# Kernel optimization log

Measured on AMD Instinct MI355X. Metric: run time of the kernel, lower is better.

## Reference

```python
import jax, jax.numpy as jnp
import numpy as np

B, D, C, F = 1024, 8192, 345, 512
PROTO_W = 0.99  # args.proto_m


def setup_inputs() -> dict:
    key = jax.random.key(0)
    k = jax.random.split(key, 6)
    img_q = jax.random.normal(k[0], (B, D), jnp.float32)
    img_q1 = jax.random.normal(k[1], (B, D), jnp.float32)
    # partial label mask: random candidate set, guarantee >=1 candidate per row
    partial_Y = (jax.random.uniform(k[2], (B, C)) < 0.3).astype(jnp.float32)
    partial_Y = partial_Y.at[jnp.arange(B), jnp.arange(B) % C].set(1.0)
    W_enc = jax.random.normal(k[3], (D, F), jnp.float32) / np.sqrt(D).astype(np.float32)
    W_fc = jax.random.normal(k[4], (F, C), jnp.float32) / np.sqrt(F).astype(np.float32)
    b_fc = jnp.zeros((C,), jnp.float32)
    proto = jax.random.normal(k[5], (C, F), jnp.float32)
    proto = proto / jnp.linalg.norm(proto, axis=1, keepdims=True)
    return {"img_q": img_q, "img_q1": img_q1, "partial_Y": partial_Y,
            "W_enc": W_enc, "W_fc": W_fc, "b_fc": b_fc, "proto": proto}


def reference(img_q, img_q1, partial_Y, W_enc, W_fc, b_fc, proto):
    # encoder: feats [B,F], logits [B,C] (abstracted backbone + shared fc)
    feats_q = img_q @ W_enc
    logits_q = feats_q @ W_fc + b_fc
    feats_q1 = img_q1 @ W_enc
    logits_q1 = feats_q1 @ W_fc + b_fc

    # partial-label restricted pseudo labels
    scores = jax.nn.softmax(logits_q, axis=1) * partial_Y
    scores = scores / scores.sum(axis=1, keepdims=True)
    labels = jnp.argmax(scores, axis=1)  # [B] int

    # Sequential per-sample EMA p[l] = w*p[l] + (1-w)*f, vectorized in closed form.
    # For a sample with c_after same-label samples occurring later, its final
    # contribution is (1-w)*w^c_after * f; the old prototype is scaled by w^count.
    onehot = jax.nn.one_hot(labels, C, dtype=feats_q.dtype)   # [B,C]
    cum = jnp.cumsum(onehot, axis=0)                          # inclusive counts
    occ = cum[jnp.arange(B), labels] - 1.0                    # occurrences before i
    total = cum[-1]                                           # [C] per-class counts
    c_after = total[labels] - occ - 1.0                       # [B]
    coef = (1.0 - PROTO_W) * PROTO_W ** c_after               # [B]
    contrib = jax.ops.segment_sum(coef[:, None] * feats_q, labels, num_segments=C)
    new_proto = (PROTO_W ** total)[:, None] * proto + contrib
    new_proto = new_proto / jnp.linalg.norm(new_proto, axis=1, keepdims=True)

    prot_scores = new_proto @ W_fc + b_fc
    return logits_q, logits_q1, new_proto, prot_scores, labels, feats_q, feats_q1
```

## Files before the change

kernel.cpp:

```cpp
#include <hip/hip_runtime.h>
#include <float.h>
#include <math.h>

#define B_SZ 1024
#define D_SZ 8192
#define C_SZ 345
#define F_SZ 512
#define PROTO_W 0.99f


#define WS_XH 0
#define WS_XL 33554432u
#define WS_WH 67108864u
#define WS_WL 75497472u
#define WS_P  83886080u
#define WS2_WFH 100663296u
#define WS2_WFL 101056512u
#define WS2_LAB 101449728u
#define WS2_NEED 101457920u

#define WS_NEED 92274688u
#define WS_FH  0u
#define WS_FL  2097152u
#define WS_WFH 4194304u
#define WS_WFL 4587520u
#define WS_NPH 4980736u
#define WS_NPL 5373952u

typedef short bf16x8 __attribute__((ext_vector_type(8)));
typedef short short4v __attribute__((ext_vector_type(4)));
typedef short short8v __attribute__((ext_vector_type(8)));
typedef float f32x4  __attribute__((ext_vector_type(4)));

__device__ __forceinline__ void split_bf16(float x, short& hi, short& lo) {
    unsigned u = __float_as_uint(x);
    unsigned r = (u + 0x7FFFu + ((u >> 16) & 1u)) >> 16;
    hi = (short)r;
    float hf = __uint_as_float(r << 16);
    lo = (short)(__float_as_uint(x - hf) >> 16);
}
__device__ __forceinline__ float bf16_f32(short h) {
    return __uint_as_float(((unsigned)(unsigned short)h) << 16);
}

__device__ __forceinline__ void gl_lds16(const short* g, short* l) {
    __builtin_amdgcn_global_load_lds(
        (const __attribute__((address_space(1))) void*)g,
        (__attribute__((address_space(3))) void*)l, 16, 0, 0);
}

__device__ __forceinline__ unsigned f2key(float v) {
    unsigned u = __float_as_uint(v);
    return (u & 0x80000000u) ? ~u : (u | 0x80000000u);
}

__device__ __forceinline__ void fence_barrier() {
    asm volatile("" ::: "memory");
    __builtin_amdgcn_s_barrier();
    asm volatile("" ::: "memory");
}

#define MFMA_BF16 __builtin_amdgcn_mfma_f32_16x16x32_bf16

#define MFMA_BLOCK(IA0, IA1, IB0, IB1)                                   \
    do {                                                                 \
        bf16x8 a0h = *(const bf16x8*)&sAh[IA0];                          \
        bf16x8 a1h = *(const bf16x8*)&sAh[IA1];                          \
        bf16x8 b0h = *(const bf16x8*)&sBh[IB0];                          \
        bf16x8 b1h = *(const bf16x8*)&sBh[IB1];                          \
        bf16x8 a0l = *(const bf16x8*)&sAl[IA0];                          \
        bf16x8 a1l = *(const bf16x8*)&sAl[IA1];                          \
        bf16x8 b0l = *(const bf16x8*)&sBl[IB0];                          \
        bf16x8 b1l = *(const bf16x8*)&sBl[IB1];                          \
        acc[0][0] = MFMA_BF16(a0h, b0h, acc[0][0], 0, 0, 0);             \
        acc[0][1] = MFMA_BF16(a0h, b1h, acc[0][1], 0, 0, 0);             \
        acc[1][0] = MFMA_BF16(a1h, b0h, acc[1][0], 0, 0, 0);             \
        acc[1][1] = MFMA_BF16(a1h, b1h, acc[1][1], 0, 0, 0);             \
        acc[0][0] = MFMA_BF16(a0h, b0l, acc[0][0], 0, 0, 0);             \
        acc[0][1] = MFMA_BF16(a0h, b1l, acc[0][1], 0, 0, 0);             \
        acc[1][0] = MFMA_BF16(a1h, b0l, acc[1][0], 0, 0, 0);             \
        acc[1][1] = MFMA_BF16(a1h, b1l, acc[1][1], 0, 0, 0);             \
        acc[0][0] = MFMA_BF16(a0l, b0h, acc[0][0], 0, 0, 0);             \
        acc[0][1] = MFMA_BF16(a0l, b1h, acc[0][1], 0, 0, 0);             \
        acc[1][0] = MFMA_BF16(a1l, b0h, acc[1][0], 0, 0, 0);             \
        acc[1][1] = MFMA_BF16(a1l, b1h, acc[1][1], 0, 0, 0);             \
    } while (0)


__global__ __launch_bounds__(256) void convert_pack2(
    const float* __restrict__ img_q, const float* __restrict__ img_q1,
    const float* __restrict__ W_enc, const float* __restrict__ W_fc,
    short* __restrict__ Ahp, short* __restrict__ Alp,
    short* __restrict__ Bhp, short* __restrict__ Blp,
    short* __restrict__ Wth, short* __restrict__ Wtl,
    unsigned long long* __restrict__ labPack)
{
    __shared__ float tile[64][65];
    const int bid = blockIdx.x;
    const int t = threadIdx.x;

    if (bid < 4)
        labPack[bid * 256 + t] = 0ull;

    if (bid < 1024) {
        const int total = 2048 * 1024;
        for (int i = bid * 256 + t; i < total; i += 1024 * 256) {
            const int row = i >> 10;
            const int cc = i & 1023;
            const float* src = (row < B_SZ)
                ? &img_q[(size_t)row * D_SZ + cc * 8]
                : &img_q1[(size_t)(row - B_SZ) * D_SZ + cc * 8];
            float4 a = ((const float4*)src)[0];
            float4 b = ((const float4*)src)[1];
            float f[8] = {a.x, a.y, a.z, a.w, b.x, b.y, b.z, b.w};
            short8v h, l;
#pragma unroll
            for (int e = 0; e < 8; ++e) {
                short hh, ll;
                split_bf16(f[e], hh, ll);
                h[e] = hh; l[e] = ll;
            }
            const int mt = row >> 7;
            const int pr = row & 127;
            const int kstep = cc >> 2;
            const int c = cc & 3;
            const int hf = pr >> 6;
            const int r = pr & 63;
            const int rp = r >> 1;
            const int slot = (((r & 1) << 2) | c) ^ (rp & 7);
            const size_t dst = (size_t)(mt * 256 + kstep) * 4096
                             + hf * 2048 + rp * 64 + slot * 8;
            *(short8v*)&Ahp[dst] = h;
            *(short8v*)&Alp[dst] = l;
        }
    } else if (bid < 2048) {
        const int id = bid - 1024;
        const int kstep64 = id >> 3;
        const int k0 = kstep64 * 64;
        const int n0 = (id & 7) * 64;
        {
            const int kr = t >> 2;
            const int cb = (t & 3) * 16;
#pragma unroll
            for (int j = 0; j < 4; ++j) {
                float4 v = *(const float4*)&W_enc[(size_t)(k0 + kr) * F_SZ + n0 + cb + j * 4];
                tile[kr][cb + j * 4 + 0] = v.x;
                tile[kr][cb + j * 4 + 1] = v.y;
                tile[kr][cb + j * 4 + 2] = v.z;
                tile[kr][cb + j * 4 + 3] = v.w;
            }
        }
        __syncthreads();
        const int n = t >> 2;
#pragma unroll
        for (int cc2 = 0; cc2 < 2; ++cc2) {
            const int ch = (t & 3) * 2 + cc2;
            short8v h, l;
#pragma unroll
            for (int e = 0; e < 8; ++e) {
                short hh, ll;
                split_bf16(tile[ch * 8 + e][n], hh, ll);
                h[e] = hh; l[e] = ll;
            }
            const int nrow = n0 + n;
            const int k32 = kstep64 * 2 + (ch >> 2);
            const int c = ch & 3;
            const int nt_ = nrow >> 7;
            const int pr = nrow & 127;
            const int hf = pr >> 6;
            const int r = pr & 63;
            const int rp = r >> 1;
            const int slot = (((r & 1) << 2) | c) ^ (rp & 7);
            const size_t dst = (size_t)(nt_ * 256 + k32) * 4096
                             + hf * 2048 + rp * 64 + slot * 8;
            *(short8v*)&Bhp[dst] = h;
            *(short8v*)&Blp[dst] = l;
        }
    } else {
        const int id = bid - 2048;
        const int k0 = (id & 7) * 64;
        const int c0 = (id >> 3) * 64;
        for (int idx = t; idx < 64 * 64; idx += 256) {
            const int kr = idx >> 6;
            const int cc = idx & 63;
            tile[kr][cc] = (c0 + cc < C_SZ) ? W_fc[(size_t)(k0 + kr) * C_SZ + c0 + cc] : 0.0f;
        }
        __syncthreads();
        const int crow = t >> 2;
#pragma unroll
        for (int cc2 = 0; cc2 < 2; ++cc2) {
            const int ch = (t & 3) * 2 + cc2;
            short8v h, l;
#pragma unroll
            for (int e = 0; e < 8; ++e) {
                short hh, ll;
                split_bf16(tile[ch * 8 + e][crow], hh, ll);
                h[e] = hh; l[e] = ll;
            }
            size_t off = (size_t)(c0 + crow) * F_SZ + k0 + ch * 8;
            *(short8v*)&Wth[off] = h;
            *(short8v*)&Wtl[off] = l;
        }
    }
}

#define V5_MFMA(PAH, PAL, PBH, PBL)                                          \
    do {                                                                     \
        bf16x8 ah[4], al[4], bh_[2], bl_[2];                                 \
        _Pragma("unroll")                                                    \
        for (int f = 0; f < 4; ++f) {                                        \
            ah[f] = *(const bf16x8*)&(PAH)[aoff[f]];                         \
            al[f] = *(const bf16x8*)&(PAL)[aoff[f]];                         \
        }                                                                    \
        _Pragma("unroll")                                                    \
        for (int g = 0; g < 2; ++g) {                                        \
            bh_[g] = *(const bf16x8*)&(PBH)[boff[g]];                        \
            bl_[g] = *(const bf16x8*)&(PBL)[boff[g]];                        \
        }                                                                    \
        __builtin_amdgcn_s_setprio(1);                                       \
        _Pragma("unroll")                                                    \
        for (int f = 0; f < 4; ++f)                                          \
            _Pragma("unroll")                                                \
            for (int g = 0; g < 2; ++g)                                      \
                acc[f][g] = MFMA_BF16(ah[f], bh_[g], acc[f][g], 0, 0, 0);    \
        _Pragma("unroll")                                                    \
        for (int f = 0; f < 4; ++f)                                          \
            _Pragma("unroll")                                                \
            for (int g = 0; g < 2; ++g)                                      \
                acc[f][g] = MFMA_BF16(ah[f], bl_[g], acc[f][g], 0, 0, 0);    \
        _Pragma("unroll")                                                    \
        for (int f = 0; f < 4; ++f)                                          \
            _Pragma("unroll")                                                \
            for (int g = 0; g < 2; ++g)                                      \
                acc[f][g] = MFMA_BF16(al[f], bh_[g], acc[f][g], 0, 0, 0);    \
        __builtin_amdgcn_s_setprio(0);                                       \
    } while (0)

#define V5_STEP(BI, SD, SW, VMLIT)                                           \
    do {                                                                     \
        asm volatile("s_waitcnt vmcnt(" VMLIT ")" ::: "memory");             \
        fence_barrier();                                                     \
        {                                                                    \
            const short* gg = gsrc0 + (size_t)(SW) * 4096;                   \
            gl_lds16(gg, SD);                                                \
            gl_lds16(gg + 512, (SD) + 512);                                  \
            gl_lds16(gg + 1024, (SD) + 1024);                                \
            gl_lds16(gg + 1536, (SD) + 1536);                                \
        }                                                                    \
        V5_MFMA(SAh[BI], SAl[BI], SBh[BI], SBl[BI]);                         \
    } while (0)

#define V5_STEPN(BI, VMLIT)                                                  \
    do {                                                                     \
        asm volatile("s_waitcnt vmcnt(" VMLIT ")" ::: "memory");             \
        fence_barrier();                                                     \
        V5_MFMA(SAh[BI], SAl[BI], SBh[BI], SBl[BI]);                         \
    } while (0)

__global__ __launch_bounds__(512, 1) void gemm_ws128_v5(
    const short* __restrict__ Ahp, const short* __restrict__ Alp,
    const short* __restrict__ Bhp, const short* __restrict__ Blp,
    float* __restrict__ P)
{
    __shared__ __align__(16) short SAh[4][4096];
    __shared__ __align__(16) short SAl[4][4096];
    __shared__ __align__(16) short SBh[4][4096];
    __shared__ __align__(16) short SBl[4][4096];

    const int t = threadIdx.x;
    const int lane = t & 63;
    const int wave = t >> 6;

    const int flat = blockIdx.x + 4 * blockIdx.y + 64 * blockIdx.z;
    const int logical = (flat & 7) * 32 + (flat >> 3);
    const int nt = logical & 3;
    const int mt = (logical >> 2) & 15;
    const int ks = logical >> 6;

    const int m0 = mt * 128;
    const int n0 = nt * 128;

    const int arr = wave >> 1;
    const int half = wave & 1;
    const short* gtile =
        (arr == 0) ? Ahp + (size_t)(mt * 256) * 4096 :
        (arr == 1) ? Alp + (size_t)(mt * 256) * 4096 :
        (arr == 2) ? Bhp + (size_t)(nt * 256) * 4096 :
                     Blp + (size_t)(nt * 256) * 4096;
    const short* gsrc0 = gtile + (size_t)(ks * 64) * 4096 + half * 2048 + lane * 8;

    short* abase =
        (arr == 0) ? &SAh[0][0] : (arr == 1) ? &SAl[0][0] :
        (arr == 2) ? &SBh[0][0] : &SBl[0][0];
    short* sd0 = abase + 0 * 4096 + half * 2048;
    short* sd1 = abase + 1 * 4096 + half * 2048;
    short* sd2 = abase + 2 * 4096 + half * 2048;
    short* sd3 = abase + 3 * 4096 + half * 2048;

    const int wr = wave >> 2;
    const int wc = wave & 3;
    const int mo = wr * 64;
    const int no = wc * 32;
    const int lr = lane & 15;
    const int lkg = lane >> 4;
    int aoff[4], boff[2];
#pragma unroll
    for (int f = 0; f < 4; ++f) {
        const int R = mo + 16 * f + lr;
        const int r = R & 63;
        const int rp = r >> 1;
        aoff[f] = (R >> 6) * 2048 + rp * 64
                + (((((r & 1) << 2) | lkg)) ^ (rp & 7)) * 8;
    }
#pragma unroll
    for (int g = 0; g < 2; ++g) {
        const int R = no + 16 * g + lr;
        const int r = R & 63;
        const int rp = r >> 1;
        boff[g] = (R >> 6) * 2048 + rp * 64
                + (((((r & 1) << 2) | lkg)) ^ (rp & 7)) * 8;
    }

    f32x4 acc[4][2] = {};

    {
        gl_lds16(gsrc0,        sd0);
        gl_lds16(gsrc0 + 512,  sd0 + 512);
        gl_lds16(gsrc0 + 1024, sd0 + 1024);
        gl_lds16(gsrc0 + 1536, sd0 + 1536);
        const short* g1 = gsrc0 + 4096;
        gl_lds16(g1,        sd1);
        gl_lds16(g1 + 512,  sd1 + 512);
        gl_lds16(g1 + 1024, sd1 + 1024);
        gl_lds16(g1 + 1536, sd1 + 1536);
        const short* g2 = gsrc0 + 8192;
        gl_lds16(g2,        sd2);
        gl_lds16(g2 + 512,  sd2 + 512);
        gl_lds16(g2 + 1024, sd2 + 1024);
        gl_lds16(g2 + 1536, sd2 + 1536);
    }

    for (int s4 = 0; s4 < 15; ++s4) {
        const int sb = s4 * 4;
        V5_STEP(0, sd3, sb + 3, "8");
        V5_STEP(1, sd0, sb + 4, "8");
        V5_STEP(2, sd1, sb + 5, "8");
        V5_STEP(3, sd2, sb + 6, "8");
    }
    V5_STEP (0, sd3, 63, "8");
    V5_STEPN(1, "8");
    V5_STEPN(2, "4");
    V5_STEPN(3, "0");

    float* Pout = P + (size_t)ks * (2048u * 512u);
#pragma unroll
    for (int f = 0; f < 4; ++f)
#pragma unroll
        for (int g = 0; g < 2; ++g) {
            const int col  = n0 + no + 16 * g + (lane & 15);
            const int row0 = m0 + mo + 16 * f + (lane >> 4) * 4;
#pragma unroll
            for (int r = 0; r < 4; ++r)
                Pout[(size_t)(row0 + r) * F_SZ + col] = acc[f][g][r];
        }
}

__global__ __launch_bounds__(256) void reduce_feats4(
    const float* __restrict__ P, float* __restrict__ feats,
    short* __restrict__ Fh, short* __restrict__ Fl)
{
    const int i4 = blockIdx.x * 256 + threadIdx.x;
    float4 a = ((const float4*)P)[i4];
#pragma unroll
    for (int sl = 1; sl < 4; ++sl) {
        float4 b = ((const float4*)(P + (size_t)sl * (2048u * 512u)))[i4];
        a.x += b.x; a.y += b.y; a.z += b.z; a.w += b.w;
    }
    ((float4*)feats)[i4] = a;
    float v[4] = {a.x, a.y, a.z, a.w};
    short4v h, l;
    short hh, ll;
#pragma unroll
    for (int e = 0; e < 4; ++e) {
        split_bf16(v[e], hh, ll); h[e] = hh; l[e] = ll;
    }
    ((short4v*)Fh)[i4] = h;
    ((short4v*)Fl)[i4] = l;
}

__global__ __launch_bounds__(256, 2) void fc_logits3(
    const short* __restrict__ Ah, const short* __restrict__ Al,
    const short* __restrict__ Bh_g, const short* __restrict__ Bl_g,
    const float* __restrict__ bias, const float* __restrict__ partial_Y,
    float* __restrict__ logits, unsigned long long* __restrict__ labPack)
{
    __shared__ __align__(16) short dAh[2][4096];
    __shared__ __align__(16) short dAl[2][4096];
    __shared__ __align__(16) short dBh[2][4096];
    __shared__ __align__(16) short dBl[2][4096];

    const int t = threadIdx.x;
    const int lane = t & 63;
    const int wave = t >> 6;
    const int n0 = blockIdx.x * 64;
    const int m0 = blockIdx.y * 64;

    const int lrow8 = lane >> 3;
    const int colOff = ((lane & 7) ^ lrow8) * 8;

    const short* gsrc = (wave == 0) ? Ah : (wave == 1) ? Al
                      : (wave == 2) ? Bh_g : Bl_g;
    const int rbase = (wave < 2) ? m0 : n0;
    short* lb[2];
    lb[0] = (wave == 0) ? dAh[0] : (wave == 1) ? dAl[0] : (wave == 2) ? dBh[0] : dBl[0];
    lb[1] = (wave == 0) ? dAh[1] : (wave == 1) ? dAl[1] : (wave == 2) ? dBh[1] : dBl[1];
    const short* gbase = gsrc + (size_t)(rbase + lrow8) * F_SZ + colOff;

    const int mo = (wave >> 1) * 32;
    const int no = (wave & 1) * 32;
    const int lr = lane & 15;
    const int lkg = lane >> 4;
    const int x7 = lr & 7;
    const int sl0 = (0 + lkg) ^ x7;
    const int sl1 = (4 + lkg) ^ x7;
    const int ra0 = (mo + lr) * 64,      ra1 = (mo + 16 + lr) * 64;
    const int rb0 = (no + lr) * 64,      rb1 = (no + 16 + lr) * 64;
    const int a00 = ra0 + sl0 * 8, a01 = ra0 + sl1 * 8;
    const int a10 = ra1 + sl0 * 8, a11 = ra1 + sl1 * 8;
    const int b00 = rb0 + sl0 * 8, b01 = rb0 + sl1 * 8;
    const int b10 = rb1 + sl0 * 8, b11 = rb1 + sl1 * 8;

    f32x4 acc[2][2] = {};

#pragma unroll
    for (int j = 0; j < 8; ++j)
        gl_lds16(gbase + (size_t)(8 * j) * F_SZ, lb[0] + j * 512);

    int buf = 0;
    for (int s = 0; s < 8; ++s) {
        if (s + 1 < 8) {
            short* dst = lb[buf ^ 1];
            const short* g = gbase + (s + 1) * 64;
#pragma unroll
            for (int j = 0; j < 8; ++j)
                gl_lds16(g + (size_t)(8 * j) * F_SZ, dst + j * 512);
            asm volatile("s_waitcnt vmcnt(8)" ::: "memory");
        } else {
            asm volatile("s_waitcnt vmcnt(0)" ::: "memory");
        }
        fence_barrier();
        __builtin_amdgcn_s_setprio(1);
        {
            const short* sAh = dAh[buf];
            const short* sAl = dAl[buf];
            const short* sBh = dBh[buf];
            const short* sBl = dBl[buf];
            MFMA_BLOCK(a00, a10, b00, b10);
            MFMA_BLOCK(a01, a11, b01, b11);
        }
        __builtin_amdgcn_s_setprio(0);
        fence_barrier();
        buf ^= 1;
    }

    const bool doArg = (m0 < B_SZ);
#pragma unroll
    for (int f = 0; f < 2; ++f) {
#pragma unroll
        for (int r = 0; r < 4; ++r) {
            const int row = m0 + mo + f * 16 + (lane >> 4) * 4 + r;
            unsigned long long best = 0;
#pragma unroll
            for (int g = 0; g < 2; ++g) {
                const int col = n0 + no + g * 16 + (lane & 15);
                if (col < C_SZ) {
                    const float v = acc[f][g][r] + bias[col];
                    logits[(size_t)row * C_SZ + col] = v;
                    if (doArg && partial_Y[(size_t)row * C_SZ + col] != 0.0f) {
                        unsigned long long p = ((unsigned long long)f2key(v) << 32)
                                             | (unsigned long long)(0xFFFFFFFFu - (unsigned)col);
                        if (p > best) best = p;
                    }
                }
            }
            if (doArg) {
#pragma unroll
                for (int m = 1; m < 16; m <<= 1) {
                    unsigned long long o = __shfl_xor(best, m);
                    if (o > best) best = o;
                }
                if ((lane & 15) == 0 && best != 0)
                    atomicMax(&labPack[row], best);
            }
        }
    }
}

__global__ __launch_bounds__(512) void proto_scores_fused(
    const unsigned long long* __restrict__ labPack,
    const float* __restrict__ feats_q,
    const float* __restrict__ proto,
    const short* __restrict__ Wth, const short* __restrict__ Wtl,
    const float* __restrict__ b_fc,
    float* __restrict__ new_proto, float* __restrict__ scores,
    float* __restrict__ labels_f)
{
    __shared__ int rowlist[B_SZ];
    __shared__ int mcount_s;
    __shared__ float nprow[F_SZ];
    __shared__ float red[8];
    __shared__ float rinv_s;
    const int c = blockIdx.x;
    const int t = threadIdx.x;
    const int lane = t & 63;
    const int w = t >> 6;

    if (c == 0) {
#pragma unroll
        for (int j = 0; j < 2; ++j) {
            const int i = t + j * 512;
            int li = (int)(0xFFFFFFFFu - (unsigned)(labPack[i] & 0xFFFFFFFFull));
            labels_f[i] = (float)li;
        }
    }

    if (w == 0) {
        int k = 0;
#pragma unroll
        for (int ch = 0; ch < 16; ++ch) {
            unsigned long long pk = labPack[ch * 64 + lane];
            int li = (int)(0xFFFFFFFFu - (unsigned)(pk & 0xFFFFFFFFull));
            unsigned long long mask = __ballot(li == c);
            if (lane == 0) {
                while (mask) {
                    int p = __builtin_ctzll(mask);
                    mask &= mask - 1;
                    rowlist[k++] = ch * 64 + p;
                }
            }
            k = __shfl(k, 0);
        }
        if (lane == 0) mcount_s = k;
    }
    __syncthreads();
    const int m = mcount_s;

    float val = proto[(size_t)c * F_SZ + t];
    for (int k = 0; k < m; ++k)
        val = PROTO_W * val + (1.0f - PROTO_W) * feats_q[(size_t)rowlist[k] * F_SZ + t];

    float sq = val * val;
#pragma unroll
    for (int off = 32; off; off >>= 1) sq += __shfl_down(sq, off);
    if ((t & 63) == 0) red[t >> 6] = sq;
    __syncthreads();
    if (t == 0) {
        float s = 0.0f;
#pragma unroll
        for (int ww = 0; ww < 8; ++ww) s += red[ww];
        rinv_s = 1.0f / sqrtf(s);
    }
    __syncthreads();
    const float v = val * rinv_s;
    new_proto[(size_t)c * F_SZ + t] = v;
    nprow[t] = v;
    __syncthreads();

    float np8[8];
#pragma unroll
    for (int j = 0; j < 8; ++j) np8[j] = nprow[lane * 8 + j];
    for (int col = w; col < C_SZ; col += 8) {
        const short8v h = *(const short8v*)&Wth[(size_t)col * F_SZ + lane * 8];
        const short8v l = *(const short8v*)&Wtl[(size_t)col * F_SZ + lane * 8];
        float p = 0.0f;
#pragma unroll
        for (int j = 0; j < 8; ++j)
            p += np8[j] * (bf16_f32(h[j]) + bf16_f32(l[j]));
#pragma unroll
        for (int off = 32; off; off >>= 1) p += __shfl_down(p, off);
        if (lane == 0) scores[(size_t)c * C_SZ + col] = p + b_fc[col];
    }
}

__global__ __launch_bounds__(256) void convert_all(
    const float* __restrict__ img_q, const float* __restrict__ img_q1,
    const float* __restrict__ W_enc, const float* __restrict__ W_fc,
    short* __restrict__ Xh, short* __restrict__ Xl,
    short* __restrict__ Wh, short* __restrict__ Wl,
    short* __restrict__ Wth, short* __restrict__ Wtl,
    unsigned long long* __restrict__ labPack)
{
    __shared__ float tile[64][65];
    const int bid = blockIdx.x;
    const int t = threadIdx.x;

    if (labPack && bid < 4)
        labPack[bid * 256 + t] = 0ull;

    if (bid < 1024) {
        const int HALF = (B_SZ * D_SZ) / 4;
        const int total = 2 * HALF;
        for (int i4 = bid * 256 + t; i4 < total; i4 += 1024 * 256) {
            float4 v = (i4 < HALF) ? ((const float4*)img_q)[i4]
                                   : ((const float4*)img_q1)[i4 - HALF];
            short4v h, l;
            short hh, ll;
            split_bf16(v.x, hh, ll); h.x = hh; l.x = ll;
            split_bf16(v.y, hh, ll); h.y = hh; l.y = ll;
            split_bf16(v.z, hh, ll); h.z = hh; l.z = ll;
            split_bf16(v.w, hh, ll); h.w = hh; l.w = ll;
            ((short4v*)Xh)[i4] = h;
            ((short4v*)Xl)[i4] = l;
        }
    } else if (bid < 2048) {
        const int id = bid - 1024;
        const int k0 = (id >> 3) * 64;
        const int n0 = (id & 7) * 64;
        {
            const int kr = t >> 2;
            const int cb = (t & 3) * 16;
#pragma unroll
            for (int j = 0; j < 4; ++j) {
                float4 v = *(const float4*)&W_enc[(size_t)(k0 + kr) * F_SZ + n0 + cb + j * 4];
                tile[kr][cb + j * 4 + 0] = v.x;
                tile[kr][cb + j * 4 + 1] = v.y;
                tile[kr][cb + j * 4 + 2] = v.z;
                tile[kr][cb + j * 4 + 3] = v.w;
            }
        }
        __syncthreads();
        const int n = t >> 2;
#pragma unroll
        for (int cc = 0; cc < 2; ++cc) {
            const int ch = (t & 3) * 2 + cc;
            short8v h, l;
#pragma unroll
            for (int e = 0; e < 8; ++e) {
                short hh, ll;
                split_bf16(tile[ch * 8 + e][n], hh, ll);
                h[e] = hh; l[e] = ll;
            }
            size_t off = (size_t)(n0 + n) * D_SZ + k0 + ch * 8;
            *(short8v*)&Wh[off] = h;
            *(short8v*)&Wl[off] = l;
        }
    } else {
        const int id = bid - 2048;
        const int k0 = (id & 7) * 64;
        const int c0 = (id >> 3) * 64;
        for (int idx = t; idx < 64 * 64; idx += 256) {
            const int kr = idx >> 6;
            const int cc = idx & 63;
            tile[kr][cc] = (c0 + cc < C_SZ) ? W_fc[(size_t)(k0 + kr) * C_SZ + c0 + cc] : 0.0f;
        }
        __syncthreads();
        const int crow = t >> 2;
#pragma unroll
        for (int cc2 = 0; cc2 < 2; ++cc2) {
            const int ch = (t & 3) * 2 + cc2;
            short8v h, l;
#pragma unroll
            for (int e = 0; e < 8; ++e) {
                short hh, ll;
                split_bf16(tile[ch * 8 + e][crow], hh, ll);
                h[e] = hh; l[e] = ll;
            }
            size_t off = (size_t)(c0 + crow) * F_SZ + k0 + ch * 8;
            *(short8v*)&Wth[off] = h;
            *(short8v*)&Wtl[off] = l;
        }
    }
}

__global__ __launch_bounds__(256, 1) void gemm_ws128(
    const short* __restrict__ Xh, const short* __restrict__ Xl,
    const short* __restrict__ Wh, const short* __restrict__ Wl,
    float* __restrict__ P, int ksteps)
{
    __shared__ __align__(16) short sAh[2][8192];
    __shared__ __align__(16) short sAl[2][8192];
    __shared__ __align__(16) short sBh[2][8192];
    __shared__ __align__(16) short sBl[2][8192];

    const int t = threadIdx.x;
    const int lane = t & 63;
    const int wave = t >> 6;
    const int nt = blockIdx.x;
    const int mt = blockIdx.y;
    const int ks = blockIdx.z;
    const int m0 = mt * 128;
    const int n0 = nt * 128;
    const int kbase = ks * ksteps * 64;

    const short* gbase =
        (wave == 0) ? Xh + (size_t)m0 * D_SZ :
        (wave == 1) ? Xl + (size_t)m0 * D_SZ :
        (wave == 2) ? Wh + (size_t)n0 * D_SZ :
                      Wl + (size_t)n0 * D_SZ;
    short* lb[2];
    lb[0] = (wave == 0) ? sAh[0] : (wave == 1) ? sAl[0] : (wave == 2) ? sBh[0] : sBl[0];
    lb[1] = (wave == 0) ? sAh[1] : (wave == 1) ? sAl[1] : (wave == 2) ? sBh[1] : sBl[1];
    const int lrow8 = lane >> 3;
    const int gchunkOff = ((lane & 7) ^ lrow8) * 8;
    const short* gsrc = gbase + (size_t)lrow8 * D_SZ + kbase + gchunkOff;

    const int mo = (wave >> 1) * 64;
    const int no = (wave & 1) * 64;
    const int lr = lane & 15;
    const int lkg = lane >> 4;
    const int x7 = lr & 7;
    const int sl0 = lkg ^ x7;
    const int sl1 = (4 + lkg) ^ x7;
    int aoff[4], boff[4];
#pragma unroll
    for (int f = 0; f < 4; ++f) {
        aoff[f] = (mo + 16 * f + lr) * 64;
        boff[f] = (no + 16 * f + lr) * 64;
    }

    f32x4 acc[4][4] = {};

#pragma unroll
    for (int j = 0; j < 16; ++j)
        gl_lds16(gsrc + (size_t)(8 * j) * D_SZ, lb[0] + j * 512);

    int buf = 0;
    for (int s = 0; s < ksteps; ++s) {
        if (s + 1 < ksteps) {
            short* dst = lb[buf ^ 1];
            const short* g = gsrc + (s + 1) * 64;
#pragma unroll
            for (int j = 0; j < 16; ++j)
                gl_lds16(g + (size_t)(8 * j) * D_SZ, dst + j * 512);
            asm volatile("s_waitcnt vmcnt(16)" ::: "memory");
        } else {
            asm volatile("s_waitcnt vmcnt(0)" ::: "memory");
        }
        fence_barrier();

        __builtin_amdgcn_s_setprio(1);
        {
            const short* pAh = sAh[buf];
            const short* pAl = sAl[buf];
            const short* pBh = sBh[buf];
            const short* pBl = sBl[buf];
#pragma unroll
            for (int ksub = 0; ksub < 2; ++ksub) {
                const int sl = ksub ? sl1 : sl0;
                bf16x8 ah[4], al[4], bh[4], blo[4];
#pragma unroll
                for (int f = 0; f < 4; ++f) {
                    ah[f]  = *(const bf16x8*)&pAh[aoff[f] + sl * 8];
                    al[f]  = *(const bf16x8*)&pAl[aoff[f] + sl * 8];
                }
#pragma unroll
                for (int g = 0; g < 4; ++g) {
                    bh[g]  = *(const bf16x8*)&pBh[boff[g] + sl * 8];
                    blo[g] = *(const bf16x8*)&pBl[boff[g] + sl * 8];
                }
#pragma unroll
                for (int f = 0; f < 4; ++f)
#pragma unroll
                    for (int g = 0; g < 4; ++g)
                        acc[f][g] = MFMA_BF16(ah[f], bh[g], acc[f][g], 0, 0, 0);
#pragma unroll
                for (int f = 0; f < 4; ++f)
#pragma unroll
                    for (int g = 0; g < 4; ++g)
                        acc[f][g] = MFMA_BF16(ah[f], blo[g], acc[f][g], 0, 0, 0);
#pragma unroll
                for (int f = 0; f < 4; ++f)
#pragma unroll
                    for (int g = 0; g < 4; ++g)
                        acc[f][g] = MFMA_BF16(al[f], bh[g], acc[f][g], 0, 0, 0);
            }
        }
        __builtin_amdgcn_s_setprio(0);
        fence_barrier();
        buf ^= 1;
    }

    float* Pout = P + (size_t)ks * (2048u * 512u);
#pragma unroll
    for (int f = 0; f < 4; ++f)
#pragma unroll
        for (int g = 0; g < 4; ++g) {
            const int col  = n0 + no + 16 * g + (lane & 15);
            const int row0 = m0 + mo + 16 * f + (lane >> 4) * 4;
#pragma unroll
            for (int r = 0; r < 4; ++r)
                Pout[(size_t)(row0 + r) * F_SZ + col] = acc[f][g][r];
        }
}

__global__ __launch_bounds__(256) void reduce_feats_split(
    const float* __restrict__ P, float* __restrict__ feats,
    short* __restrict__ Fh, short* __restrict__ Fl,
    const float* __restrict__ W_fc,
    short* __restrict__ Wth, short* __restrict__ Wtl)
{
    const int bid = blockIdx.x;
    const int t = threadIdx.x;
    if (bid < 1024) {
        const int n4 = (2048 * 512) / 4;
        const float* P1 = P + 2048 * 512;
        for (int i4 = bid * 256 + t; i4 < n4; i4 += 1024 * 256) {
            float4 a = ((const float4*)P)[i4];
            float4 b = ((const float4*)P1)[i4];
            float v[4] = {a.x + b.x, a.y + b.y, a.z + b.z, a.w + b.w};
            short4v h, l;
            short hh, ll;
#pragma unroll
            for (int e = 0; e < 4; ++e) {
                feats[i4 * 4 + e] = v[e];
                split_bf16(v[e], hh, ll); h[e] = hh; l[e] = ll;
            }
            ((short4v*)Fh)[i4] = h;
            ((short4v*)Fl)[i4] = l;
        }
    } else {
        __shared__ float tile[64][65];
        const int id = bid - 1024;
        const int k0 = (id & 7) * 64;
        const int c0 = (id >> 3) * 64;
        for (int idx = t; idx < 64 * 64; idx += 256) {
            const int kr = idx >> 6;
            const int cc = idx & 63;
            tile[kr][cc] = (c0 + cc < C_SZ) ? W_fc[(size_t)(k0 + kr) * C_SZ + c0 + cc] : 0.0f;
        }
        __syncthreads();
        const int crow = t >> 2;
#pragma unroll
        for (int cc2 = 0; cc2 < 2; ++cc2) {
            const int ch = (t & 3) * 2 + cc2;
            short8v h, l;
#pragma unroll
            for (int e = 0; e < 8; ++e) {
                short hh, ll;
                split_bf16(tile[ch * 8 + e][crow], hh, ll);
                h[e] = hh; l[e] = ll;
            }
            size_t off = (size_t)(c0 + crow) * F_SZ + k0 + ch * 8;
            *(short8v*)&Wth[off] = h;
            *(short8v*)&Wtl[off] = l;
        }
    }
}

__global__ __launch_bounds__(256) void gemm_fc(
    const short* __restrict__ Ah, const short* __restrict__ Al,
    const short* __restrict__ Bh, const short* __restrict__ Bl,
    const float* __restrict__ bias, float* __restrict__ Cout, int M)
{
    __shared__ __align__(16) short sAh[4096];
    __shared__ __align__(16) short sAl[4096];
    __shared__ __align__(16) short sBh[4096];
    __shared__ __align__(16) short sBl[4096];

    const int t = threadIdx.x;
    const int lane = t & 63;
    const int wave = t >> 6;
    const int n0 = blockIdx.x * 64;
    const int m0 = blockIdx.y * 64;

    const int lrow8 = lane >> 3;
    const int colOff = ((lane & 7) ^ lrow8) * 8;

    short* lbase = (wave == 0) ? sAh : (wave == 1) ? sAl : (wave == 2) ? sBh : sBl;
    const short* gA = (wave == 1) ? Al : Ah;
    const short* gB = (wave == 3) ? Bl : Bh;
    const bool isA = wave < 2;

    const int mo = (wave >> 1) * 32;
    const int no = (wave & 1) * 32;
    const int lr = lane & 15;
    const int lkg = lane >> 4;
    const int x7 = lr & 7;
    const int sl0 = (0 + lkg) ^ x7;
    const int sl1 = (4 + lkg) ^ x7;
    const int ra0 = (mo + lr) * 64,      ra1 = (mo + 16 + lr) * 64;
    const int rb0 = (no + lr) * 64,      rb1 = (no + 16 + lr) * 64;
    const int a00 = ra0 + sl0 * 8, a01 = ra0 + sl1 * 8;
    const int a10 = ra1 + sl0 * 8, a11 = ra1 + sl1 * 8;
    const int b00 = rb0 + sl0 * 8, b01 = rb0 + sl1 * 8;
    const int b10 = rb1 + sl0 * 8, b11 = rb1 + sl1 * 8;

    f32x4 acc[2][2] = {};

    for (int s = 0; s < 8; ++s) {
        __syncthreads();
        if (isA) {
#pragma unroll
            for (int j = 0; j < 8; ++j) {
                int row = m0 + lrow8 + 8 * j;
                if (row > M - 1) row = M - 1;
                gl_lds16(gA + (size_t)row * F_SZ + s * 64 + colOff, lbase + j * 512);
            }
        } else {
#pragma unroll
            for (int j = 0; j < 8; ++j) {
                int row = n0 + lrow8 + 8 * j;
                gl_lds16(gB + (size_t)row * F_SZ + s * 64 + colOff, lbase + j * 512);
            }
        }
        __syncthreads();
        MFMA_BLOCK(a00, a10, b00, b10);
        MFMA_BLOCK(a01, a11, b01, b11);
    }

#pragma unroll
    for (int f = 0; f < 2; ++f)
#pragma unroll
        for (int g = 0; g < 2; ++g) {
            const int col  = n0 + no + g * 16 + (lane & 15);
            if (col >= C_SZ) continue;
            const float bb = bias[col];
            const int row0 = m0 + mo + f * 16 + (lane >> 4) * 4;
#pragma unroll
            for (int r = 0; r < 4; ++r) {
                const int row = row0 + r;
                if (row < M)
                    Cout[(size_t)row * C_SZ + col] = acc[f][g][r] + bb;
            }
        }
}

__global__ __launch_bounds__(64) void argmax_labels(
    const float* __restrict__ logits, const float* __restrict__ partial_Y,
    float* __restrict__ labels_f)
{
    const int i = blockIdx.x;
    const int lane = threadIdx.x;
    float best = -FLT_MAX;
    int bidx = C_SZ;
    for (int c = lane; c < C_SZ; c += 64) {
        if (partial_Y[(size_t)i * C_SZ + c] != 0.0f) {
            float v = logits[(size_t)i * C_SZ + c];
            if (v > best || (v == best && c < bidx)) { best = v; bidx = c; }
        }
    }
#pragma unroll
    for (int off = 32; off; off >>= 1) {
        float ov = __shfl_down(best, off);
        int oi = __shfl_down(bidx, off);
        if (ov > best || (ov == best && oi < bidx)) { best = ov; bidx = oi; }
    }
    if (lane == 0) labels_f[i] = (float)bidx;
}

__global__ __launch_bounds__(512) void proto_update(
    const float* __restrict__ labels_f, const float* __restrict__ feats_q,
    const float* __restrict__ proto, float* __restrict__ new_proto,
    short* __restrict__ NPh, short* __restrict__ NPl)
{
    __shared__ int lab[B_SZ];
    __shared__ float red[8];
    __shared__ float rinv_s;
    const int c = blockIdx.x;
    const int t = threadIdx.x;
    for (int i = t; i < B_SZ; i += 512) lab[i] = (int)labels_f[i];
    __syncthreads();
    float val = proto[(size_t)c * F_SZ + t];
    for (int i = 0; i < B_SZ; ++i) {
        if (lab[i] == c)
            val = PROTO_W * val + (1.0f - PROTO_W) * feats_q[(size_t)i * F_SZ + t];
    }
    float sq = val * val;
#pragma unroll
    for (int off = 32; off; off >>= 1) sq += __shfl_down(sq, off);
    if ((t & 63) == 0) red[t >> 6] = sq;
    __syncthreads();
    if (t == 0) {
        float s = 0.0f;
#pragma unroll
        for (int w = 0; w < 8; ++w) s += red[w];
        rinv_s = 1.0f / sqrtf(s);
    }
    __syncthreads();
    const float v = val * rinv_s;
    new_proto[(size_t)c * F_SZ + t] = v;
    if (NPh) {
        short hh, ll;
        split_bf16(v, hh, ll);
        NPh[(size_t)c * F_SZ + t] = hh;
        NPl[(size_t)c * F_SZ + t] = ll;
    }
}

extern "C" void kernel_launch(void* const* d_in, const int* in_sizes, int n_in,
                              void* d_out, int out_size, void* d_ws, size_t ws_size,
                              hipStream_t stream)
{
    const float* img_q     = (const float*)d_in[0];
    const float* img_q1    = (const float*)d_in[1];
    const float* partial_Y = (const float*)d_in[2];
    const float* W_enc     = (const float*)d_in[3];
    const float* W_fc      = (const float*)d_in[4];
    const float* b_fc      = (const float*)d_in[5];
    const float* proto     = (const float*)d_in[6];

    float* out       = (float*)d_out;
    float* logits    = out;
    float* new_proto = out + 706560;
    float* scores    = out + 883200;
    float* labels_f  = out + 1002225;
    float* feats     = out + 1003249;

    char* ws = (char*)d_ws;
    short* Xh = (short*)(ws + WS_XH);
    short* Xl = (short*)(ws + WS_XL);
    short* Wh = (short*)(ws + WS_WH);
    short* Wl = (short*)(ws + WS_WL);
    float* P  = (float*)(ws + WS_P);

    if (ws_size >= (size_t)WS2_NEED) {
        short* Wth = (short*)(ws + WS2_WFH);
        short* Wtl = (short*)(ws + WS2_WFL);
        unsigned long long* labPack = (unsigned long long*)(ws + WS2_LAB);
        short* Fh = (short*)(ws + 0u);
        short* Fl = (short*)(ws + 2097152u);

        hipLaunchKernelGGL(convert_pack2, dim3(2096), dim3(256), 0, stream,
                           img_q, img_q1, W_enc, W_fc, Xh, Xl, Wh, Wl, Wth, Wtl,
                           labPack);
        hipLaunchKernelGGL(gemm_ws128_v5, dim3(4, 16, 4), dim3(512), 0, stream,
                           Xh, Xl, Wh, Wl, P);
        hipLaunchKernelGGL(reduce_feats4, dim3(1024), dim3(256), 0, stream,
                           P, feats, Fh, Fl);
        hipLaunchKernelGGL(fc_logits3, dim3(6, 32), dim3(256), 0, stream,
                           Fh, Fl, Wth, Wtl, b_fc, partial_Y, logits, labPack);
        hipLaunchKernelGGL(proto_scores_fused, dim3(345), dim3(512), 0, stream,
                           labPack, feats, proto, Wth, Wtl, b_fc,
                           new_proto, scores, labels_f);
    } else {
        short* Fh  = (short*)(ws + WS_FH);
        short* Fl  = (short*)(ws + WS_FL);
        short* Wth = (short*)(ws + WS_WFH);
        short* Wtl = (short*)(ws + WS_WFL);
        short* NPh = (short*)(ws + WS_NPH);
        short* NPl = (short*)(ws + WS_NPL);

        hipLaunchKernelGGL(convert_all, dim3(2048), dim3(256), 0, stream,
                           img_q, img_q1, W_enc, W_fc, Xh, Xl, Wh, Wl,
                           (short*)nullptr, (short*)nullptr,
                           (unsigned long long*)nullptr);
        hipLaunchKernelGGL(gemm_ws128, dim3(4, 16, 2), dim3(256), 0, stream,
                           Xh, Xl, Wh, Wl, P, 64);
        hipLaunchKernelGGL(reduce_feats_split, dim3(1072), dim3(256), 0, stream,
                           P, feats, Fh, Fl, W_fc, Wth, Wtl);
        hipLaunchKernelGGL(gemm_fc, dim3(6, 32), dim3(256), 0, stream,
                           Fh, Fl, Wth, Wtl, b_fc, logits, 2048);
        hipLaunchKernelGGL(argmax_labels, dim3(1024), dim3(64), 0, stream,
                           logits, partial_Y, labels_f);
        hipLaunchKernelGGL(proto_update, dim3(345), dim3(512), 0, stream,
                           labels_f, feats, proto, new_proto, NPh, NPl);
        hipLaunchKernelGGL(gemm_fc, dim3(6, 6), dim3(256), 0, stream,
                           NPh, NPl, Wth, Wtl, b_fc, scores, C_SZ);
    }
}
```

Before: 242.6 us.

## Fuse split-K reduction into GEMM and bf16 splitting into FC logits kernel

```diff
diff --git a/kernel.cpp b/kernel.cpp
--- a/kernel.cpp
+++ b/kernel.cpp
@@ -257,10 +257,11 @@
         V5_MFMA(SAh[BI], SAl[BI], SBh[BI], SBl[BI]);                         \
     } while (0)
 
-__global__ __launch_bounds__(512, 1) void gemm_ws128_v5(
+__global__ __launch_bounds__(512, 1) void gemm_ws128_v6(
     const short* __restrict__ Ahp, const short* __restrict__ Alp,
     const short* __restrict__ Bhp, const short* __restrict__ Blp,
-    float* __restrict__ P)
+    float* __restrict__ P, float* __restrict__ feats,
+    unsigned long long* __restrict__ tileCnt)
 {
     __shared__ __align__(16) short SAh[4][4096];
     __shared__ __align__(16) short SAl[4][4096];
@@ -363,33 +364,36 @@
             for (int r = 0; r < 4; ++r)
                 Pout[(size_t)(row0 + r) * F_SZ + col] = acc[f][g][r];
         }
-}
-
-__global__ __launch_bounds__(256) void reduce_feats4(
-    const float* __restrict__ P, float* __restrict__ feats,
-    short* __restrict__ Fh, short* __restrict__ Fl)
-{
-    const int i4 = blockIdx.x * 256 + threadIdx.x;
-    float4 a = ((const float4*)P)[i4];
-#pragma unroll
-    for (int sl = 1; sl < 4; ++sl) {
-        float4 b = ((const float4*)(P + (size_t)sl * (2048u * 512u)))[i4];
-        a.x += b.x; a.y += b.y; a.z += b.z; a.w += b.w;
-    }
-    ((float4*)feats)[i4] = a;
-    float v[4] = {a.x, a.y, a.z, a.w};
-    short4v h, l;
-    short hh, ll;
-#pragma unroll
-    for (int e = 0; e < 4; ++e) {
-        split_bf16(v[e], hh, ll); h[e] = hh; l[e] = ll;
-    }
-    ((short4v*)Fh)[i4] = h;
-    ((short4v*)Fl)[i4] = l;
-}
-
-__global__ __launch_bounds__(256, 2) void fc_logits3(
-    const short* __restrict__ Ah, const short* __restrict__ Al,
+
+    asm volatile("s_waitcnt vmcnt(0)" ::: "memory");
+    __threadfence();
+    __syncthreads();
+    if (t == 0) {
+        unsigned long long old = atomicAdd(&tileCnt[mt * 4 + nt], 1ull);
+        *(int*)&SAh[0][0] = (old == 3ull) ? 1 : 0;
+    }
+    __syncthreads();
+    if (*(int*)&SAh[0][0]) {
+        __threadfence();
+#pragma unroll
+        for (int q = 0; q < 8; ++q) {
+            const int idx = t + q * 512;
+            const int row = idx >> 5;
+            const int ch = idx & 31;
+            const size_t g = (size_t)(m0 + row) * F_SZ + n0 + ch * 4;
+            float4 v = *(const float4*)&P[g];
+#pragma unroll
+            for (int sl = 1; sl < 4; ++sl) {
+                float4 b = *(const float4*)&P[(size_t)sl * (2048u * 512u) + g];
+                v.x += b.x; v.y += b.y; v.z += b.z; v.w += b.w;
+            }
+            *(float4*)&feats[g] = v;
+        }
+    }
+}
+
+__global__ __launch_bounds__(256, 2) void fc_logits4(
+    const float* __restrict__ feats,
     const short* __restrict__ Bh_g, const short* __restrict__ Bl_g,
     const float* __restrict__ bias, const float* __restrict__ partial_Y,
     float* __restrict__ logits, unsigned long long* __restrict__ labPack)
@@ -406,15 +410,16 @@
     const int m0 = blockIdx.y * 64;
 
     const int lrow8 = lane >> 3;
-    const int colOff = ((lane & 7) ^ lrow8) * 8;
-
-    const short* gsrc = (wave == 0) ? Ah : (wave == 1) ? Al
-                      : (wave == 2) ? Bh_g : Bl_g;
-    const int rbase = (wave < 2) ? m0 : n0;
-    short* lb[2];
-    lb[0] = (wave == 0) ? dAh[0] : (wave == 1) ? dAl[0] : (wave == 2) ? dBh[0] : dBl[0];
-    lb[1] = (wave == 0) ? dAh[1] : (wave == 1) ? dAl[1] : (wave == 2) ? dBh[1] : dBl[1];
-    const short* gbase = gsrc + (size_t)(rbase + lrow8) * F_SZ + colOff;
+    const int cg = (lane & 7) ^ lrow8;
+    const bool isA = (wave < 2);
+
+    const short* gB = (wave == 2) ? Bh_g : Bl_g;
+    short* lbB[2];
+    lbB[0] = (wave == 2) ? dBh[0] : dBl[0];
+    lbB[1] = (wave == 2) ? dBh[1] : dBl[1];
+    const short* gbaseB = gB + (size_t)(n0 + lrow8) * F_SZ + cg * 8;
+
+    const float* gA0 = feats + (size_t)(m0 + lrow8 + 8 * (wave * 4)) * F_SZ + cg * 8;
 
     const int mo = (wave >> 1) * 32;
     const int no = (wave & 1) * 32;
@@ -432,21 +437,54 @@
 
     f32x4 acc[2][2] = {};
 
-#pragma unroll
-    for (int j = 0; j < 8; ++j)
-        gl_lds16(gbase + (size_t)(8 * j) * F_SZ, lb[0] + j * 512);
+    if (isA) {
+#pragma unroll
+        for (int j2 = 0; j2 < 4; ++j2) {
+            const float* src = gA0 + (size_t)(8 * j2) * F_SZ;
+            float4 v0 = ((const float4*)src)[0];
+            float4 v1 = ((const float4*)src)[1];
+            float f8[8] = {v0.x, v0.y, v0.z, v0.w, v1.x, v1.y, v1.z, v1.w};
+            bf16x8 h, l;
+#pragma unroll
+            for (int e = 0; e < 8; ++e) {
+                short hh, ll;
+                split_bf16(f8[e], hh, ll);
+                h[e] = hh; l[e] = ll;
+            }
+            const int j = wave * 4 + j2;
+            *(bf16x8*)&dAh[0][j * 512 + lane * 8] = h;
+            *(bf16x8*)&dAl[0][j * 512 + lane * 8] = l;
+        }
+        asm volatile("s_waitcnt lgkmcnt(0)" ::: "memory");
+    } else {
+#pragma unroll
+        for (int j = 0; j < 8; ++j)
+            gl_lds16(gbaseB + (size_t)(8 * j) * F_SZ, lbB[0] + j * 512);
+    }
 
     int buf = 0;
     for (int s = 0; s < 8; ++s) {
-        if (s + 1 < 8) {
-            short* dst = lb[buf ^ 1];
-            const short* g = gbase + (s + 1) * 64;
-#pragma unroll
-            for (int j = 0; j < 8; ++j)
-                gl_lds16(g + (size_t)(8 * j) * F_SZ, dst + j * 512);
-            asm volatile("s_waitcnt vmcnt(8)" ::: "memory");
+        float4 ra[4][2];
+        if (isA) {
+            if (s + 1 < 8) {
+#pragma unroll
+                for (int j2 = 0; j2 < 4; ++j2) {
+                    const float* src = gA0 + (size_t)(8 * j2) * F_SZ + (s + 1) * 64;
+                    ra[j2][0] = ((const float4*)src)[0];
+                    ra[j2][1] = ((const float4*)src)[1];
+                }
+            }
         } else {
-            asm volatile("s_waitcnt vmcnt(0)" ::: "memory");
+            if (s + 1 < 8) {
+                short* dst = lbB[buf ^ 1];
+                const short* g = gbaseB + (s + 1) * 64;
+#pragma unroll
+                for (int j = 0; j < 8; ++j)
+                    gl_lds16(g + (size_t)(8 * j) * F_SZ, dst + j * 512);
+                asm volatile("s_waitcnt vmcnt(8)" ::: "memory");
+            } else {
+                asm volatile("s_waitcnt vmcnt(0)" ::: "memory");
+            }
         }
         fence_barrier();
         __builtin_amdgcn_s_setprio(1);
@@ -459,6 +497,25 @@
             MFMA_BLOCK(a01, a11, b01, b11);
         }
         __builtin_amdgcn_s_setprio(0);
+        if (isA && s + 1 < 8) {
+            asm volatile("s_waitcnt vmcnt(0)" ::: "memory");
+#pragma unroll
+            for (int j2 = 0; j2 < 4; ++j2) {
+                float f8[8] = {ra[j2][0].x, ra[j2][0].y, ra[j2][0].z, ra[j2][0].w,
+                               ra[j2][1].x, ra[j2][1].y, ra[j2][1].z, ra[j2][1].w};
+                bf16x8 h, l;
+#pragma unroll
+                for (int e = 0; e < 8; ++e) {
+                    short hh, ll;
+                    split_bf16(f8[e], hh, ll);
+                    h[e] = hh; l[e] = ll;
+                }
+                const int j = wave * 4 + j2;
+                *(bf16x8*)&dAh[buf ^ 1][j * 512 + lane * 8] = h;
+                *(bf16x8*)&dAl[buf ^ 1][j * 512 + lane * 8] = l;
+            }
+            asm volatile("s_waitcnt lgkmcnt(0)" ::: "memory");
+        }
         fence_barrier();
         buf ^= 1;
     }
@@ -1017,18 +1074,14 @@
         short* Wth = (short*)(ws + WS2_WFH);
         short* Wtl = (short*)(ws + WS2_WFL);
         unsigned long long* labPack = (unsigned long long*)(ws + WS2_LAB);
-        short* Fh = (short*)(ws + 0u);
-        short* Fl = (short*)(ws + 2097152u);
 
         hipLaunchKernelGGL(convert_pack2, dim3(2096), dim3(256), 0, stream,
                            img_q, img_q1, W_enc, W_fc, Xh, Xl, Wh, Wl, Wth, Wtl,
                            labPack);
-        hipLaunchKernelGGL(gemm_ws128_v5, dim3(4, 16, 4), dim3(512), 0, stream,
-                           Xh, Xl, Wh, Wl, P);
-        hipLaunchKernelGGL(reduce_feats4, dim3(1024), dim3(256), 0, stream,
-                           P, feats, Fh, Fl);
-        hipLaunchKernelGGL(fc_logits3, dim3(6, 32), dim3(256), 0, stream,
-                           Fh, Fl, Wth, Wtl, b_fc, partial_Y, logits, labPack);
+        hipLaunchKernelGGL(gemm_ws128_v6, dim3(4, 16, 4), dim3(512), 0, stream,
+                           Xh, Xl, Wh, Wl, P, feats, labPack);
+        hipLaunchKernelGGL(fc_logits4, dim3(6, 32), dim3(256), 0, stream,
+                           feats, Wth, Wtl, b_fc, partial_Y, logits, labPack);
         hipLaunchKernelGGL(proto_scores_fused, dim3(345), dim3(512), 0, stream,
                            labPack, feats, proto, Wth, Wtl, b_fc,
                            new_proto, scores, labels_f);
```

After: 316.6 us. 1.3x slower.
